# Optimization experiments

Measured on AMD Instinct MI355X. Metric: run time of the kernel, lower is better.

Reference implementation:

```python
import jax, jax.numpy as jnp
import numpy as np

N_NODES = 50000
N_EDGES = 800000
IN_CH = 128
HID = 128


def setup_inputs() -> dict:
    key = jax.random.key(0)
    ks = jax.random.split(key, 8)
    s = 0.05
    x = jax.random.normal(ks[0], (N_NODES, IN_CH), dtype=jnp.float32)
    edge_index = jax.random.randint(ks[1], (2, N_EDGES), 0, N_NODES, dtype=jnp.int64)
    W1l = jax.random.normal(ks[2], (IN_CH, HID), dtype=jnp.float32) * s
    W1r = jax.random.normal(ks[3], (IN_CH, HID), dtype=jnp.float32) * s
    b1 = jnp.zeros((HID,), dtype=jnp.float32)
    W2l = jax.random.normal(ks[4], (HID, HID), dtype=jnp.float32) * s
    W2r = jax.random.normal(ks[5], (HID, HID), dtype=jnp.float32) * s
    b2 = jnp.zeros((HID,), dtype=jnp.float32)
    Wout = jax.random.normal(ks[6], (HID, 2), dtype=jnp.float32) * s
    bout = jnp.zeros((2,), dtype=jnp.float32)
    return {"x": x, "edge_index": edge_index, "W1l": W1l, "W1r": W1r, "b1": b1,
            "W2l": W2l, "W2r": W2r, "b2": b2, "Wout": Wout, "bout": bout}


def _mean_aggr(h, src, dst, n_nodes):
    # mean of neighbor (source) features per destination node (PyG SAGEConv default)
    msg_sum = jax.ops.segment_sum(h[src], dst, num_segments=n_nodes)  # [N, D]
    deg = jax.ops.segment_sum(jnp.ones((src.shape[0],), dtype=h.dtype), dst,
                              num_segments=n_nodes)  # [N]
    return msg_sum / jnp.maximum(deg, 1.0)[:, None]


def _sage_conv(h, src, dst, Wl, Wr, b, n_nodes):
    aggr = _mean_aggr(h, src, dst, n_nodes)
    return aggr @ Wl + h @ Wr + b


def reference(x, edge_index, W1l, W1r, b1, W2l, W2r, b2, Wout, bout):
    n = x.shape[0]
    src, dst = edge_index[0], edge_index[1]
    h = jax.nn.relu(_sage_conv(x, src, dst, W1l, W1r, b1, n))
    # dropout is identity in inference mode
    h = jax.nn.relu(_sage_conv(h, src, dst, W2l, W2r, b2, n))
    logits = h @ Wout + bout
    return (logits, h)
```

## Files before the change

### kernel.cpp

```cpp
#include <hip/hip_runtime.h>

#define NN 50000
#define NE 800000
#define CH 128
#define CAP 64
#define PSTRIDE 6256

#define EPT2 2
#define EDGE_GRID ((NE + 256 * EPT2 - 1) / (256 * EPT2))
#define WTP_BLK 256
#define CAST_BLK ((NN * (CH / 2) / 4 + 255) / 256)

typedef __attribute__((ext_vector_type(8))) short short8;
typedef __attribute__((ext_vector_type(4))) float float4a;
typedef __attribute__((ext_vector_type(4))) float fltx4;
typedef __attribute__((ext_vector_type(4))) unsigned untx4;

#define DEG_OFF  0
#define CSR_OFF  50048
#define XB_OFF   1650048
#define AGB_OFF  4850048
#define H1B_OFF  8050048
#define WTP_OFF  11250048

static __device__ __forceinline__ unsigned short f2b(float f) {
    unsigned u = __float_as_uint(f);
    unsigned r = u + 0x7fff + ((u >> 16) & 1);
    return (unsigned short)(r >> 16);
}

static __device__ __forceinline__ void edge_one(
    int src, int dst, int* __restrict__ deg,
    unsigned short* __restrict__ csr) {
    if ((unsigned)dst < NN && (unsigned)src < NN) {
        int p = dst & 7;
        int r = atomicAdd(&deg[p * PSTRIDE + (dst >> 3)], 1);
        r = min(r, CAP - 1);
        csr[(size_t)dst * CAP + r] = (unsigned short)src;
    }
}

__global__ __launch_bounds__(256) void k_edge(
    const int* __restrict__ eidx, int* __restrict__ deg,
    unsigned short* __restrict__ csr) {
    int e0 = (blockIdx.x * 256 + threadIdx.x) * EPT2;
    if (e0 >= NE) return;
    int2 s = *(const int2*)(eidx + e0);
    int2 d = *(const int2*)(eidx + NE + e0);
    edge_one(s.x, d.x, deg, csr);
    edge_one(s.y, d.y, deg, csr);
}

__global__ __launch_bounds__(256) void k_prep(
    const float* __restrict__ W1l, const float* __restrict__ W1r,
    const float* __restrict__ W2l, const float* __restrict__ W2r,
    unsigned short* __restrict__ wtp,
    const float* __restrict__ x, unsigned* __restrict__ xb) {
    int b = blockIdx.x;
    if (b < WTP_BLK) {
        int i = b * 256 + threadIdx.x;
        int layer = i >> 15;
        int li = i & 32767;
        int e = li & 7, lane = (li >> 3) & 63, j = (li >> 9) & 7, kt = li >> 12;
        int ln = lane & 15, quad = lane >> 4;
        int n = j * 16 + ln;
        int k = kt * 32 + quad * 8 + e;
        const float* Wl = layer ? W2l : W1l;
        const float* Wr = layer ? W2r : W1r;
        float v = (k < 128) ? Wl[k * 128 + n] : Wr[(k - 128) * 128 + n];
        __builtin_nontemporal_store(f2b(v), &wtp[(size_t)layer * 32768 + li]);
    } else {
        int gid = (b - WTP_BLK) * 256 + threadIdx.x;
        if (gid < NN * (CH / 2) / 4) {
            fltx4 v0 = __builtin_nontemporal_load((const fltx4*)x + gid * 2);
            fltx4 v1 = __builtin_nontemporal_load((const fltx4*)x + gid * 2 + 1);
            untx4 o;
            o.x = (unsigned)f2b(v0.x) | ((unsigned)f2b(v0.y) << 16);
            o.y = (unsigned)f2b(v0.z) | ((unsigned)f2b(v0.w) << 16);
            o.z = (unsigned)f2b(v1.x) | ((unsigned)f2b(v1.y) << 16);
            o.w = (unsigned)f2b(v1.z) | ((unsigned)f2b(v1.w) << 16);
            __builtin_nontemporal_store(o, (untx4*)xb + gid);
        }
    }
}

static __device__ __forceinline__ void acc8(float* acc, uint4 v) {
    acc[0] += __uint_as_float(v.x << 16); acc[1] += __uint_as_float(v.x & 0xffff0000u);
    acc[2] += __uint_as_float(v.y << 16); acc[3] += __uint_as_float(v.y & 0xffff0000u);
    acc[4] += __uint_as_float(v.z << 16); acc[5] += __uint_as_float(v.z & 0xffff0000u);
    acc[6] += __uint_as_float(v.w << 16); acc[7] += __uint_as_float(v.w & 0xffff0000u);
}

__global__ __launch_bounds__(256) void k_gather4(
    const int* __restrict__ deg, const unsigned short* __restrict__ csr,
    const uint4* __restrict__ featb, uint4* __restrict__ aggrb) {
    int wave = (blockIdx.x * 256 + threadIdx.x) >> 6;
    int lane = threadIdx.x & 63;
    if (wave >= NN) return;
    int d = min(deg[(wave & 7) * PSTRIDE + (wave >> 3)], CAP);
    const unsigned short* row = csr + (size_t)wave * CAP;
    int g = lane >> 4;
    int c = lane & 15;

    float acc[8];
    #pragma unroll
    for (int e = 0; e < 8; ++e) acc[e] = 0.0f;

    int i0 = 0;
    for (; i0 + 16 <= d; i0 += 16) {
        int s1 = row[i0 + g];
        int s2 = row[i0 + 4 + g];
        int s3 = row[i0 + 8 + g];
        int s4 = row[i0 + 12 + g];
        uint4 v1 = featb[(size_t)s1 * 16 + c];
        uint4 v2 = featb[(size_t)s2 * 16 + c];
        uint4 v3 = featb[(size_t)s3 * 16 + c];
        uint4 v4 = featb[(size_t)s4 * 16 + c];
        acc8(acc, v1); acc8(acc, v2); acc8(acc, v3); acc8(acc, v4);
    }
    for (; i0 + 8 <= d; i0 += 8) {
        int s1 = row[i0 + g];
        int s2 = row[i0 + 4 + g];
        uint4 v1 = featb[(size_t)s1 * 16 + c];
        uint4 v2 = featb[(size_t)s2 * 16 + c];
        acc8(acc, v1); acc8(acc, v2);
    }
    if (i0 < d) {
        int n1 = i0 + g, n2 = i0 + 4 + g;
        int s1 = (n1 < d) ? (int)row[n1] : 0;
        int s2 = (n2 < d) ? (int)row[n2] : 0;
        uint4 v1 = featb[(size_t)s1 * 16 + c];
        uint4 v2 = featb[(size_t)s2 * 16 + c];
        if (n1 < d) acc8(acc, v1);
        if (n2 < d) acc8(acc, v2);
    }

    #pragma unroll
    for (int e = 0; e < 8; ++e) {
        acc[e] += __shfl_xor(acc[e], 32, 64);
        acc[e] += __shfl_xor(acc[e], 16, 64);
    }
    if (lane < 16) {
        float s = 1.0f / (float)(d > 1 ? d : 1);
        uint4 o;
        o.x = (unsigned)f2b(acc[0] * s) | ((unsigned)f2b(acc[1] * s) << 16);
        o.y = (unsigned)f2b(acc[2] * s) | ((unsigned)f2b(acc[3] * s) << 16);
        o.z = (unsigned)f2b(acc[4] * s) | ((unsigned)f2b(acc[5] * s) << 16);
        o.w = (unsigned)f2b(acc[6] * s) | ((unsigned)f2b(acc[7] * s) << 16);
        aggrb[(size_t)wave * 16 + c] = o;
    }
}

template <bool BF16OUT>
__global__ __launch_bounds__(256) void k_layer_mfma(
    const short* __restrict__ aggrb, const short* __restrict__ hinb,
    const short* __restrict__ wtp, const float* __restrict__ bias,
    float* __restrict__ outf, unsigned short* __restrict__ outb,
    const float* __restrict__ Wout, const float* __restrict__ bout,
    float* __restrict__ logits) {
    int lane = threadIdx.x & 63;
    int wid = threadIdx.x >> 6;
    int m0 = blockIdx.x * 64 + wid * 16;
    int ln = lane & 15;
    int quad = lane >> 4;
    int m = m0 + ln;
    int mc = min(m, NN - 1);

    float4a acc[8];
    #pragma unroll
    for (int j = 0; j < 8; ++j) acc[j] = (float4a){0.0f, 0.0f, 0.0f, 0.0f};

    #pragma unroll
    for (int kt = 0; kt < 8; ++kt) {
        const short* arow = (kt < 4 ? aggrb : hinb) + (size_t)mc * CH + (kt & 3) * 32 + quad * 8;
        short8 av = *(const short8*)arow;
        const short* bk = wtp + (size_t)kt * 4096 + lane * 8;
        #pragma unroll
        for (int j = 0; j < 8; ++j) {
            short8 bv = *(const short8*)(bk + j * 512);
            acc[j] = __builtin_amdgcn_mfma_f32_16x16x32_bf16(av, bv, acc[j], 0, 0, 0);
        }
    }

    float p0[4], p1[4];
    #pragma unroll
    for (int r = 0; r < 4; ++r) { p0[r] = 0.0f; p1[r] = 0.0f; }

    #pragma unroll
    for (int j = 0; j < 8; ++j) {
        int col = j * 16 + ln;
        float bj = bias[col];
        float w0 = 0.0f, w1 = 0.0f;
        if (!BF16OUT) { w0 = Wout[col * 2]; w1 = Wout[col * 2 + 1]; }
        #pragma unroll
        for (int r = 0; r < 4; ++r) {
            int row = m0 + quad * 4 + r;
            float v = fmaxf(acc[j][r] + bj, 0.0f);
            if (row < NN) {
                if (BF16OUT) outb[(size_t)row * CH + col] = f2b(v);
                else         outf[(size_t)row * CH + col] = v;
            }
            if (!BF16OUT) { p0[r] = fmaf(v, w0, p0[r]); p1[r] = fmaf(v, w1, p1[r]); }
        }
    }

    if (!BF16OUT) {
        #pragma unroll
        for (int r = 0; r < 4; ++r) {
            #pragma unroll
            for (int off = 1; off < 16; off <<= 1) {
                p0[r] += __shfl_xor(p0[r], off, 64);
                p1[r] += __shfl_xor(p1[r], off, 64);
            }
        }
        if (ln == 0) {
            float b0 = bout[0], b1 = bout[1];
            #pragma unroll
            for (int r = 0; r < 4; ++r) {
                int row = m0 + quad * 4 + r;
                if (row < NN) {
                    logits[row * 2 + 0] = p0[r] + b0;
                    logits[row * 2 + 1] = p1[r] + b1;
                }
            }
        }
    }
}

extern "C" void kernel_launch(void* const* d_in, const int* in_sizes, int n_in,
                              void* d_out, int out_size, void* d_ws, size_t ws_size,
                              hipStream_t stream) {
    const float* x    = (const float*)d_in[0];
    const int*   eidx = (const int*)d_in[1];
    const float* W1l  = (const float*)d_in[2];
    const float* W1r  = (const float*)d_in[3];
    const float* b1   = (const float*)d_in[4];
    const float* W2l  = (const float*)d_in[5];
    const float* W2r  = (const float*)d_in[6];
    const float* b2   = (const float*)d_in[7];
    const float* Wout = (const float*)d_in[8];
    const float* bout = (const float*)d_in[9];

    float* out    = (float*)d_out;
    float* ws     = (float*)d_ws;
    int*   deg    = (int*)ws;
    unsigned short* csr = (unsigned short*)(ws + CSR_OFF);
    unsigned* xb  = (unsigned*)(ws + XB_OFF);
    unsigned* agb = (unsigned*)(ws + AGB_OFF);
    unsigned* h1b = (unsigned*)(ws + H1B_OFF);
    unsigned short* wtp = (unsigned short*)(ws + WTP_OFF);
    float* logits = out;
    float* hout   = out + 100000;

    (void)hipMemsetAsync(deg, 0, 8 * PSTRIDE * sizeof(int), stream);

    k_edge<<<EDGE_GRID, 256, 0, stream>>>(eidx, deg, csr);
    k_prep<<<WTP_BLK + CAST_BLK, 256, 0, stream>>>(W1l, W1r, W2l, W2r, wtp, x, xb);

    k_gather4<<<(NN + 3) / 4, 256, 0, stream>>>(deg, csr, (const uint4*)xb, (uint4*)agb);
    k_layer_mfma<true><<<(NN + 63) / 64, 256, 0, stream>>>(
        (const short*)agb, (const short*)xb, (const short*)wtp, b1,
        nullptr, (unsigned short*)h1b, nullptr, nullptr, nullptr);

    k_gather4<<<(NN + 3) / 4, 256, 0, stream>>>(deg, csr, (const uint4*)h1b, (uint4*)agb);
    k_layer_mfma<false><<<(NN + 63) / 64, 256, 0, stream>>>(
        (const short*)agb, (const short*)h1b, (const short*)(wtp + 32768), b2,
        hout, nullptr, Wout, bout, logits);
}
```

Before: 254.7 us.

## Build CSR via per-block LDS histograms, column scan, and placement pass

Replaces the global-atomic edge bucketing with a three-kernel scheme. Each of 256 blocks counts its edge slice into a 16-bit-packed LDS histogram, a scan kernel turns these into per-block offsets and degrees, and a placement kernel recomputes ranks in LDS to write CSR slots. The aim is to remove contended global atomics and the memset. The cost is two extra launches, reading the edge list twice, and a scan that walks 256 rows of 25000 words. The 100KB LDS histogram limits each CU to one block, and the workspace reuses the aggregation buffer.

After: 251.1 us. Within noise of the previous version (-1.4%).

```diff
diff --git a/kernel.cpp b/kernel.cpp
--- a/kernel.cpp
+++ b/kernel.cpp
@@ -4,10 +4,11 @@
 #define NE 800000
 #define CH 128
 #define CAP 64
-#define PSTRIDE 6256
-
-#define EPT2 2
-#define EDGE_GRID ((NE + 256 * EPT2 - 1) / (256 * EPT2))
+
+#define NBLK 256
+#define EPB (NE / NBLK)
+#define HWORDS (NN / 2)
+
 #define WTP_BLK 256
 #define CAST_BLK ((NN * (CH / 2) / 4 + 255) / 256)
 
@@ -22,6 +23,7 @@
 #define AGB_OFF  4850048
 #define H1B_OFF  8050048
 #define WTP_OFF  11250048
+#define BH_OFF   AGB_OFF
 
 static __device__ __forceinline__ unsigned short f2b(float f) {
     unsigned u = __float_as_uint(f);
@@ -29,26 +31,62 @@
     return (unsigned short)(r >> 16);
 }
 
-static __device__ __forceinline__ void edge_one(
-    int src, int dst, int* __restrict__ deg,
+__global__ __launch_bounds__(256) void k_count(
+    const int* __restrict__ eidx, unsigned* __restrict__ bh) {
+    __shared__ unsigned h[HWORDS];
+    for (int i = threadIdx.x; i < HWORDS; i += 256) h[i] = 0;
+    __syncthreads();
+    int b = blockIdx.x;
+    const int* srcp = eidx + (size_t)b * EPB;
+    const int* dstp = eidx + NE + (size_t)b * EPB;
+    for (int i = threadIdx.x; i < EPB; i += 256) {
+        int s = srcp[i];
+        int d = dstp[i];
+        if ((unsigned)d < NN && (unsigned)s < NN)
+            atomicAdd(&h[d >> 1], 1u << ((d & 1) * 16));
+    }
+    __syncthreads();
+    unsigned* out = bh + (size_t)b * HWORDS;
+    for (int i = threadIdx.x; i < HWORDS; i += 256) out[i] = h[i];
+}
+
+__global__ __launch_bounds__(256) void k_scan(
+    unsigned* __restrict__ bh, int* __restrict__ deg) {
+    int i = blockIdx.x * 256 + threadIdx.x;
+    if (i >= HWORDS) return;
+    unsigned lo = 0, hi = 0;
+    for (int b = 0; b < NBLK; ++b) {
+        unsigned v = bh[(size_t)b * HWORDS + i];
+        bh[(size_t)b * HWORDS + i] = lo | (hi << 16);
+        lo += v & 0xffffu;
+        hi += v >> 16;
+    }
+    deg[i * 2]     = (int)lo;
+    deg[i * 2 + 1] = (int)hi;
+}
+
+__global__ __launch_bounds__(256) void k_place(
+    const int* __restrict__ eidx, const unsigned* __restrict__ bh,
     unsigned short* __restrict__ csr) {
-    if ((unsigned)dst < NN && (unsigned)src < NN) {
-        int p = dst & 7;
-        int r = atomicAdd(&deg[p * PSTRIDE + (dst >> 3)], 1);
-        r = min(r, CAP - 1);
-        csr[(size_t)dst * CAP + r] = (unsigned short)src;
-    }
-}
-
-__global__ __launch_bounds__(256) void k_edge(
-    const int* __restrict__ eidx, int* __restrict__ deg,
-    unsigned short* __restrict__ csr) {
-    int e0 = (blockIdx.x * 256 + threadIdx.x) * EPT2;
-    if (e0 >= NE) return;
-    int2 s = *(const int2*)(eidx + e0);
-    int2 d = *(const int2*)(eidx + NE + e0);
-    edge_one(s.x, d.x, deg, csr);
-    edge_one(s.y, d.y, deg, csr);
+    __shared__ unsigned h[HWORDS];
+    for (int i = threadIdx.x; i < HWORDS; i += 256) h[i] = 0;
+    __syncthreads();
+    int b = blockIdx.x;
+    const int* srcp = eidx + (size_t)b * EPB;
+    const int* dstp = eidx + NE + (size_t)b * EPB;
+    const unsigned* base = bh + (size_t)b * HWORDS;
+    for (int i = threadIdx.x; i < EPB; i += 256) {
+        int s = srcp[i];
+        int d = dstp[i];
+        if ((unsigned)d < NN && (unsigned)s < NN) {
+            int sh = (d & 1) * 16;
+            unsigned prev = atomicAdd(&h[d >> 1], 1u << sh);
+            unsigned rank = (prev >> sh) & 0xffffu;
+            unsigned bs = (base[d >> 1] >> sh) & 0xffffu;
+            int slot = min((int)(bs + rank), CAP - 1);
+            csr[(size_t)d * CAP + slot] = (unsigned short)s;
+        }
+    }
 }
 
 __global__ __launch_bounds__(256) void k_prep(
@@ -97,7 +135,7 @@
     int wave = (blockIdx.x * 256 + threadIdx.x) >> 6;
     int lane = threadIdx.x & 63;
     if (wave >= NN) return;
-    int d = min(deg[(wave & 7) * PSTRIDE + (wave >> 3)], CAP);
+    int d = min(deg[wave], CAP);
     const unsigned short* row = csr + (size_t)wave * CAP;
     int g = lane >> 4;
     int c = lane & 15;
@@ -248,13 +286,15 @@
     unsigned* xb  = (unsigned*)(ws + XB_OFF);
     unsigned* agb = (unsigned*)(ws + AGB_OFF);
     unsigned* h1b = (unsigned*)(ws + H1B_OFF);
+    unsigned* bh  = (unsigned*)(ws + BH_OFF);
     unsigned short* wtp = (unsigned short*)(ws + WTP_OFF);
     float* logits = out;
     float* hout   = out + 100000;
 
-    (void)hipMemsetAsync(deg, 0, 8 * PSTRIDE * sizeof(int), stream);
-
-    k_edge<<<EDGE_GRID, 256, 0, stream>>>(eidx, deg, csr);
+    k_count<<<NBLK, 256, 0, stream>>>(eidx, bh);
+    k_scan<<<(HWORDS + 255) / 256, 256, 0, stream>>>(bh, deg);
+    k_place<<<NBLK, 256, 0, stream>>>(eidx, bh, csr);
+
     k_prep<<<WTP_BLK + CAST_BLK, 256, 0, stream>>>(W1l, W1r, W2l, W2r, wtp, x, xb);
 
     k_gather4<<<(NN + 3) / 4, 256, 0, stream>>>(deg, csr, (const uint4*)xb, (uint4*)agb);
```
